# Kernel optimization log

Hardware: AMD Instinct MI355X
Metric: run time of the kernel (lower is better)

The kernel has to match this reference:

```python
import jax, jax.numpy as jnp
import numpy as np

N, F, H, F_ = 8192, 256, 2, 64
NEG_MASK = -1e10
LEAKY_SLOPE = 0.2


def setup_inputs() -> dict:
    key = jax.random.key(0)
    k0, k1, k2, k3 = jax.random.split(key, 4)
    X = jax.random.normal(k0, (N, F), jnp.float32)
    A = (jax.random.uniform(k1, (N, N)) < 0.01).astype(jnp.float32)
    A = jnp.maximum(A, jnp.eye(N, dtype=jnp.float32))
    W = jax.random.normal(k2, (H, F, F_), jnp.float32) * (1.0 / np.sqrt(F))
    b = jnp.zeros((H, F_), jnp.float32)
    a = jax.random.normal(k3, (H, F_), jnp.float32) * 0.1
    return {"X": X, "A": A, "W": W, "b": b, "a": a}


def reference(X, A, W, b, a):
    # per-head projected features: [H, N, F_]
    feats = jnp.einsum('nf,hfo->hno', X, W)
    # score[h,i,j] = sum_o feats[h,i,o] * feats[h,j,o] * a[h,o]
    # (identical math to Dot(axes=-1)([X_0*X_1, a^T]) without the [N,N,F_] tensor)
    scores = jnp.einsum('hno,hmo->hnm', feats * a[:, None, :], feats)
    scores = jax.nn.leaky_relu(scores, negative_slope=LEAKY_SLOPE)
    scores = scores + NEG_MASK * (1.0 - A)  # adjacency mask (broadcast over heads)
    attn = jax.nn.softmax(scores, axis=-1)  # [H, N, N]
    # dropout_rate=0 -> identity at inference
    out = jnp.einsum('hnm,hmo->hno', attn, feats) + b[:, None, :]  # [H, N, F_]
    out = jnp.transpose(out, (1, 0, 2)).reshape(X.shape[0], H * F_)  # concat heads
    return jax.nn.relu(out)
```

## Files before the change

kernel.cpp:

```cpp
#include <hip/hip_runtime.h>

#define NN 8192
#define FIN 256
#define FO 64
#define CAP 192

typedef float nf4 __attribute__((ext_vector_type(4)));

__global__ __launch_bounds__(256) void feats_kernel(
    const float* __restrict__ X,
    const float* __restrict__ W,
    float* __restrict__ feats)
{
    __shared__ float Ws[128*FO];
    __shared__ float Xs[32*132];
    const int h = blockIdx.y;
    const int row0 = blockIdx.x * 32;
    const int t = threadIdx.x;
    const int rg = t >> 4;
    const int c0 = (t & 15) << 2;
    float acc0[4] = {0.f,0.f,0.f,0.f};
    float acc1[4] = {0.f,0.f,0.f,0.f};

    for (int kp = 0; kp < 2; ++kp){
        const int kb = kp * 128;
        const float* Wh = W + h*FIN*FO + kb*FO;
        #pragma unroll
        for (int it=0; it<8; ++it){
            int flat = (it*256 + t)*4;
            *(float4*)&Ws[flat] = *(const float4*)&Wh[flat];
        }
        #pragma unroll
        for (int it=0; it<4; ++it){
            int flat = (it*256 + t)*4;
            int r = flat >> 7, f0 = flat & 127;
            *(float4*)&Xs[r*132 + f0] = *(const float4*)&X[(size_t)(row0+r)*FIN + kb + f0];
        }
        __syncthreads();
        const float* xp0 = &Xs[(rg*2+0)*132];
        const float* xp1 = &Xs[(rg*2+1)*132];
        #pragma unroll 4
        for (int k=0; k<128; ++k){
            float x0 = xp0[k], x1 = xp1[k];
            float4 w4 = *(const float4*)&Ws[k*FO + c0];
            acc0[0]=fmaf(x0,w4.x,acc0[0]); acc0[1]=fmaf(x0,w4.y,acc0[1]);
            acc0[2]=fmaf(x0,w4.z,acc0[2]); acc0[3]=fmaf(x0,w4.w,acc0[3]);
            acc1[0]=fmaf(x1,w4.x,acc1[0]); acc1[1]=fmaf(x1,w4.y,acc1[1]);
            acc1[2]=fmaf(x1,w4.z,acc1[2]); acc1[3]=fmaf(x1,w4.w,acc1[3]);
        }
        __syncthreads();
    }
    float* o0 = feats + ((size_t)(row0 + rg*2 + 0)*2 + h)*FO + c0;
    float* o1 = feats + ((size_t)(row0 + rg*2 + 1)*2 + h)*FO + c0;
    *(float4*)o0 = make_float4(acc0[0],acc0[1],acc0[2],acc0[3]);
    *(float4*)o1 = make_float4(acc1[0],acc1[1],acc1[2],acc1[3]);
}

__global__ __launch_bounds__(512) void gat_kernel(
    const float* __restrict__ A,
    const float* __restrict__ feats,
    const float* __restrict__ av,
    const float* __restrict__ bv,
    float* __restrict__ out)
{
    __shared__ int   nsh[CAP];
    __shared__ float s0[CAP], s1[CAP];
    __shared__ float part[8*128];
    __shared__ float red[2];
    __shared__ int   s_c;

    const int i = blockIdx.x, t = threadIdx.x;
    const int l  = t & 63;
    const int wv = t >> 6;
    const int gi = t >> 5, l32 = t & 31;

    float4 qa = *(const float4*)&av[l32*4];
    float4 qf = *(const float4*)&feats[(size_t)i*128 + l32*4];
    const float4 q4 = make_float4(qf.x*qa.x, qf.y*qa.y, qf.z*qa.z, qf.w*qa.w);

    if (t == 0) s_c = 0;
    __syncthreads();

    const nf4* Arow4 = (const nf4*)(A + (size_t)i*NN);
    nf4 v[4];
    #pragma unroll
    for (int r=0; r<4; ++r) v[r] = __builtin_nontemporal_load(&Arow4[r*512 + t]);

    const unsigned long long ltmask = (1ull << l) - 1ull;
    #pragma unroll
    for (int r=0; r<4; ++r){
        unsigned long long m0 = __ballot(v[r].x != 0.0f);
        unsigned long long m1 = __ballot(v[r].y != 0.0f);
        unsigned long long m2 = __ballot(v[r].z != 0.0f);
        unsigned long long m3 = __ballot(v[r].w != 0.0f);
        int p0 = __popcll(m0), p1 = __popcll(m1), p2 = __popcll(m2), p3 = __popcll(m3);
        int base = 0;
        if (l == 0) base = atomicAdd(&s_c, p0+p1+p2+p3);
        base = __shfl(base, 0, 64);
        const int colb = (r*512 + t)*4;
        if ((m0>>l)&1){ int p = base + __popcll(m0 & ltmask); if (p<CAP) nsh[p] = colb;   } base += p0;
        if ((m1>>l)&1){ int p = base + __popcll(m1 & ltmask); if (p<CAP) nsh[p] = colb+1; } base += p1;
        if ((m2>>l)&1){ int p = base + __popcll(m2 & ltmask); if (p<CAP) nsh[p] = colb+2; } base += p2;
        if ((m3>>l)&1){ int p = base + __popcll(m3 & ltmask); if (p<CAP) nsh[p] = colb+3; }
    }
    __syncthreads();
    const int n = min(s_c, CAP);

    for (int k0 = gi*4; k0 < n; k0 += 64){
        const int kn = min(4, n - k0);
        float4 f[4];
        #pragma unroll
        for (int u=0; u<4; ++u){
            int j = (u < kn) ? nsh[k0+u] : i;
            f[u] = *(const float4*)&feats[(size_t)j*128 + l32*4];
        }
        #pragma unroll
        for (int u=0; u<4; ++u){
            float d = f[u].x*q4.x + f[u].y*q4.y + f[u].z*q4.z + f[u].w*q4.w;
            d += __shfl_xor(d, 1, 64);
            d += __shfl_xor(d, 2, 64);
            d += __shfl_xor(d, 4, 64);
            d += __shfl_xor(d, 8, 64);
            d = (d >= 0.f) ? d : 0.2f*d;
            if (u < kn){
                if (l32 == 0)  s0[k0+u] = d;
                if (l32 == 16) s1[k0+u] = d;
            }
        }
    }
    __syncthreads();

    if (wv < 2){
        float* ss = wv ? s1 : s0;
        float m = -1e30f;
        for (int k=l; k<n; k+=64) m = fmaxf(m, ss[k]);
        #pragma unroll
        for (int off=32; off; off>>=1) m = fmaxf(m, __shfl_xor(m, off, 64));
        float sum = 0.f;
        for (int k=l; k<n; k+=64){ float p = __expf(ss[k]-m); ss[k] = p; sum += p; }
        #pragma unroll
        for (int off=32; off; off>>=1) sum += __shfl_xor(sum, off, 64);
        if (l == 0) red[wv] = sum;
    }
    __syncthreads();

    const int g8 = t >> 6;
    const int o2 = (t & 63) * 2;
    const float* ps = (o2 >= 64) ? s1 : s0;
    float2 acc = make_float2(0.f, 0.f);
    int k = g8;
    for (; k + 24 < n; k += 32){
        int j0 = nsh[k], j1 = nsh[k+8], j2 = nsh[k+16], j3 = nsh[k+24];
        float2 f0 = *(const float2*)&feats[(size_t)j0*128 + o2];
        float2 f1 = *(const float2*)&feats[(size_t)j1*128 + o2];
        float2 f2 = *(const float2*)&feats[(size_t)j2*128 + o2];
        float2 f3 = *(const float2*)&feats[(size_t)j3*128 + o2];
        float p0 = ps[k], p1 = ps[k+8], p2 = ps[k+16], p3 = ps[k+24];
        acc.x = fmaf(p0, f0.x, acc.x); acc.y = fmaf(p0, f0.y, acc.y);
        acc.x = fmaf(p1, f1.x, acc.x); acc.y = fmaf(p1, f1.y, acc.y);
        acc.x = fmaf(p2, f2.x, acc.x); acc.y = fmaf(p2, f2.y, acc.y);
        acc.x = fmaf(p3, f3.x, acc.x); acc.y = fmaf(p3, f3.y, acc.y);
    }
    for (; k < n; k += 8){
        int j = nsh[k];
        float2 f = *(const float2*)&feats[(size_t)j*128 + o2];
        float p = ps[k];
        acc.x = fmaf(p, f.x, acc.x); acc.y = fmaf(p, f.y, acc.y);
    }
    *(float2*)&part[g8*128 + o2] = acc;
    __syncthreads();

    if (t < 128){
        float num = part[t]       + part[128+t] + part[256+t] + part[384+t]
                  + part[512+t]   + part[640+t] + part[768+t] + part[896+t];
        float val = num / red[t>>6] + bv[t];
        out[(size_t)i*128 + t] = fmaxf(val, 0.f);
    }
}

extern "C" void kernel_launch(void* const* d_in, const int* in_sizes, int n_in,
                              void* d_out, int out_size, void* d_ws, size_t ws_size,
                              hipStream_t stream) {
    const float* X = (const float*)d_in[0];
    const float* A = (const float*)d_in[1];
    const float* W = (const float*)d_in[2];
    const float* b = (const float*)d_in[3];
    const float* a = (const float*)d_in[4];
    float* out = (float*)d_out;

    float* feats = (float*)d_ws;

    feats_kernel<<<dim3(NN/32, 2), 256, 0, stream>>>(X, W, feats);
    gat_kernel  <<<dim3(NN),       512, 0, stream>>>(A, feats, a, b, out);
}
```

Before: 391.9 us.

## Process four GAT rows per block and prefetch the next adjacency row

The attention kernel now handles four consecutive rows per block, using 256 threads instead of one row per 512-thread block. While the current row's neighbour list is compacted and aggregated, the block issues non-temporal loads for the next row of A into registers, so the streaming read overlaps with compute. The aggregation phase uses float4 gathers per thread to fit the smaller block. The feats output indexing is rewritten in an equivalent form. In exchange there are four times fewer blocks, fewer threads per row and more registers per thread, which can reduce the latency hiding that parallelism across blocks used to provide.

```diff
diff --git a/kernel.cpp b/kernel.cpp
--- a/kernel.cpp
+++ b/kernel.cpp
@@ -4,6 +4,7 @@
 #define FIN 256
 #define FO 64
 #define CAP 192
+#define RPB 4
 
 typedef float nf4 __attribute__((ext_vector_type(4)));
 
@@ -50,13 +51,13 @@
         }
         __syncthreads();
     }
-    float* o0 = feats + ((size_t)(row0 + rg*2 + 0)*2 + h)*FO + c0;
-    float* o1 = feats + ((size_t)(row0 + rg*2 + 1)*2 + h)*FO + c0;
+    float* o0 = feats + (size_t)(row0 + rg*2 + 0)*128 + h*FO + c0;
+    float* o1 = feats + (size_t)(row0 + rg*2 + 1)*128 + h*FO + c0;
     *(float4*)o0 = make_float4(acc0[0],acc0[1],acc0[2],acc0[3]);
     *(float4*)o1 = make_float4(acc1[0],acc1[1],acc1[2],acc1[3]);
 }
 
-__global__ __launch_bounds__(512) void gat_kernel(
+__global__ __launch_bounds__(256) void gat_kernel(
     const float* __restrict__ A,
     const float* __restrict__ feats,
     const float* __restrict__ av,
@@ -69,112 +70,125 @@
     __shared__ float red[2];
     __shared__ int   s_c;
 
-    const int i = blockIdx.x, t = threadIdx.x;
+    const int t = threadIdx.x;
     const int l  = t & 63;
     const int wv = t >> 6;
     const int gi = t >> 5, l32 = t & 31;
-
-    float4 qa = *(const float4*)&av[l32*4];
-    float4 qf = *(const float4*)&feats[(size_t)i*128 + l32*4];
-    const float4 q4 = make_float4(qf.x*qa.x, qf.y*qa.y, qf.z*qa.z, qf.w*qa.w);
+    const int base_row = blockIdx.x * RPB;
+
+    const float4 qa = *(const float4*)&av[l32*4];
+    const unsigned long long ltmask = (1ull << l) - 1ull;
 
     if (t == 0) s_c = 0;
     __syncthreads();
 
-    const nf4* Arow4 = (const nf4*)(A + (size_t)i*NN);
-    nf4 v[4];
-    #pragma unroll
-    for (int r=0; r<4; ++r) v[r] = __builtin_nontemporal_load(&Arow4[r*512 + t]);
-
-    const unsigned long long ltmask = (1ull << l) - 1ull;
-    #pragma unroll
-    for (int r=0; r<4; ++r){
-        unsigned long long m0 = __ballot(v[r].x != 0.0f);
-        unsigned long long m1 = __ballot(v[r].y != 0.0f);
-        unsigned long long m2 = __ballot(v[r].z != 0.0f);
-        unsigned long long m3 = __ballot(v[r].w != 0.0f);
-        int p0 = __popcll(m0), p1 = __popcll(m1), p2 = __popcll(m2), p3 = __popcll(m3);
-        int base = 0;
-        if (l == 0) base = atomicAdd(&s_c, p0+p1+p2+p3);
-        base = __shfl(base, 0, 64);
-        const int colb = (r*512 + t)*4;
-        if ((m0>>l)&1){ int p = base + __popcll(m0 & ltmask); if (p<CAP) nsh[p] = colb;   } base += p0;
-        if ((m1>>l)&1){ int p = base + __popcll(m1 & ltmask); if (p<CAP) nsh[p] = colb+1; } base += p1;
-        if ((m2>>l)&1){ int p = base + __popcll(m2 & ltmask); if (p<CAP) nsh[p] = colb+2; } base += p2;
-        if ((m3>>l)&1){ int p = base + __popcll(m3 & ltmask); if (p<CAP) nsh[p] = colb+3; }
+    nf4 v[8];
+    {
+        const nf4* Ar = (const nf4*)(A + (size_t)base_row*NN);
+        #pragma unroll
+        for (int r=0; r<8; ++r) v[r] = __builtin_nontemporal_load(&Ar[r*256 + t]);
     }
-    __syncthreads();
-    const int n = min(s_c, CAP);
-
-    for (int k0 = gi*4; k0 < n; k0 += 64){
-        const int kn = min(4, n - k0);
-        float4 f[4];
-        #pragma unroll
-        for (int u=0; u<4; ++u){
-            int j = (u < kn) ? nsh[k0+u] : i;
-            f[u] = *(const float4*)&feats[(size_t)j*128 + l32*4];
-        }
-        #pragma unroll
-        for (int u=0; u<4; ++u){
-            float d = f[u].x*q4.x + f[u].y*q4.y + f[u].z*q4.z + f[u].w*q4.w;
-            d += __shfl_xor(d, 1, 64);
-            d += __shfl_xor(d, 2, 64);
-            d += __shfl_xor(d, 4, 64);
-            d += __shfl_xor(d, 8, 64);
-            d = (d >= 0.f) ? d : 0.2f*d;
-            if (u < kn){
-                if (l32 == 0)  s0[k0+u] = d;
-                if (l32 == 16) s1[k0+u] = d;
+
+    for (int rr=0; rr<RPB; ++rr){
+        const int i = base_row + rr;
+
+        float4 qf = *(const float4*)&feats[(size_t)i*128 + l32*4];
+        const float4 q4 = make_float4(qf.x*qa.x, qf.y*qa.y, qf.z*qa.z, qf.w*qa.w);
+
+        #pragma unroll
+        for (int r=0; r<8; ++r){
+            unsigned long long m0 = __ballot(v[r].x != 0.0f);
+            unsigned long long m1 = __ballot(v[r].y != 0.0f);
+            unsigned long long m2 = __ballot(v[r].z != 0.0f);
+            unsigned long long m3 = __ballot(v[r].w != 0.0f);
+            int p0 = __popcll(m0), p1 = __popcll(m1), p2 = __popcll(m2), p3 = __popcll(m3);
+            int base = 0;
+            if (l == 0) base = atomicAdd(&s_c, p0+p1+p2+p3);
+            base = __shfl(base, 0, 64);
+            const int colb = (r*256 + t)*4;
+            if ((m0>>l)&1){ int p = base + __popcll(m0 & ltmask); if (p<CAP) nsh[p] = colb;   } base += p0;
+            if ((m1>>l)&1){ int p = base + __popcll(m1 & ltmask); if (p<CAP) nsh[p] = colb+1; } base += p1;
+            if ((m2>>l)&1){ int p = base + __popcll(m2 & ltmask); if (p<CAP) nsh[p] = colb+2; } base += p2;
+            if ((m3>>l)&1){ int p = base + __popcll(m3 & ltmask); if (p<CAP) nsh[p] = colb+3; }
+        }
+        if (rr < RPB-1){
+            const nf4* An = (const nf4*)(A + (size_t)(i+1)*NN);
+            #pragma unroll
+            for (int r=0; r<8; ++r) v[r] = __builtin_nontemporal_load(&An[r*256 + t]);
+        }
+        __syncthreads();
+        const int n = min(s_c, CAP);
+
+        for (int k0 = gi*4; k0 < n; k0 += 32){
+            const int kn = min(4, n - k0);
+            float4 f[4];
+            #pragma unroll
+            for (int u=0; u<4; ++u){
+                int j = (u < kn) ? nsh[k0+u] : i;
+                f[u] = *(const float4*)&feats[(size_t)j*128 + l32*4];
             }
-        }
-    }
-    __syncthreads();
-
-    if (wv < 2){
-        float* ss = wv ? s1 : s0;
-        float m = -1e30f;
-        for (int k=l; k<n; k+=64) m = fmaxf(m, ss[k]);
-        #pragma unroll
-        for (int off=32; off; off>>=1) m = fmaxf(m, __shfl_xor(m, off, 64));
-        float sum = 0.f;
-        for (int k=l; k<n; k+=64){ float p = __expf(ss[k]-m); ss[k] = p; sum += p; }
-        #pragma unroll
-        for (int off=32; off; off>>=1) sum += __shfl_xor(sum, off, 64);
-        if (l == 0) red[wv] = sum;
-    }
-    __syncthreads();
-
-    const int g8 = t >> 6;
-    const int o2 = (t & 63) * 2;
-    const float* ps = (o2 >= 64) ? s1 : s0;
-    float2 acc = make_float2(0.f, 0.f);
-    int k = g8;
-    for (; k + 24 < n; k += 32){
-        int j0 = nsh[k], j1 = nsh[k+8], j2 = nsh[k+16], j3 = nsh[k+24];
-        float2 f0 = *(const float2*)&feats[(size_t)j0*128 + o2];
-        float2 f1 = *(const float2*)&feats[(size_t)j1*128 + o2];
-        float2 f2 = *(const float2*)&feats[(size_t)j2*128 + o2];
-        float2 f3 = *(const float2*)&feats[(size_t)j3*128 + o2];
-        float p0 = ps[k], p1 = ps[k+8], p2 = ps[k+16], p3 = ps[k+24];
-        acc.x = fmaf(p0, f0.x, acc.x); acc.y = fmaf(p0, f0.y, acc.y);
-        acc.x = fmaf(p1, f1.x, acc.x); acc.y = fmaf(p1, f1.y, acc.y);
-        acc.x = fmaf(p2, f2.x, acc.x); acc.y = fmaf(p2, f2.y, acc.y);
-        acc.x = fmaf(p3, f3.x, acc.x); acc.y = fmaf(p3, f3.y, acc.y);
-    }
-    for (; k < n; k += 8){
-        int j = nsh[k];
-        float2 f = *(const float2*)&feats[(size_t)j*128 + o2];
-        float p = ps[k];
-        acc.x = fmaf(p, f.x, acc.x); acc.y = fmaf(p, f.y, acc.y);
-    }
-    *(float2*)&part[g8*128 + o2] = acc;
-    __syncthreads();
-
-    if (t < 128){
-        float num = part[t]       + part[128+t] + part[256+t] + part[384+t]
-                  + part[512+t]   + part[640+t] + part[768+t] + part[896+t];
-        float val = num / red[t>>6] + bv[t];
-        out[(size_t)i*128 + t] = fmaxf(val, 0.f);
+            #pragma unroll
+            for (int u=0; u<4; ++u){
+                float d = f[u].x*q4.x + f[u].y*q4.y + f[u].z*q4.z + f[u].w*q4.w;
+                d += __shfl_xor(d, 1, 64);
+                d += __shfl_xor(d, 2, 64);
+                d += __shfl_xor(d, 4, 64);
+                d += __shfl_xor(d, 8, 64);
+                d = (d >= 0.f) ? d : 0.2f*d;
+                if (u < kn){
+                    if (l32 == 0)  s0[k0+u] = d;
+                    if (l32 == 16) s1[k0+u] = d;
+                }
+            }
+        }
+        __syncthreads();
+
+        if (wv < 2){
+            float* ss = wv ? s1 : s0;
+            float m = -1e30f;
+            for (int k=l; k<n; k+=64) m = fmaxf(m, ss[k]);
+            #pragma unroll
+            for (int off=32; off; off>>=1) m = fmaxf(m, __shfl_xor(m, off, 64));
+            float sum = 0.f;
+            for (int k=l; k<n; k+=64){ float p = __expf(ss[k]-m); ss[k] = p; sum += p; }
+            #pragma unroll
+            for (int off=32; off; off>>=1) sum += __shfl_xor(sum, off, 64);
+            if (l == 0) red[wv] = sum;
+        }
+        if (t == 192) s_c = 0;
+        __syncthreads();
+
+        const int o4 = l32*4;
+        const float* ps = (l32 >= 16) ? s1 : s0;
+        float4 acc = make_float4(0.f,0.f,0.f,0.f);
+        int k = gi;
+        for (; k + 24 < n; k += 32){
+            int j0 = nsh[k], j1 = nsh[k+8], j2 = nsh[k+16], j3 = nsh[k+24];
+            float4 f0 = *(const float4*)&feats[(size_t)j0*128 + o4];
+            float4 f1 = *(const float4*)&feats[(size_t)j1*128 + o4];
+            float4 f2 = *(const float4*)&feats[(size_t)j2*128 + o4];
+            float4 f3 = *(const float4*)&feats[(size_t)j3*128 + o4];
+            float p0 = ps[k], p1 = ps[k+8], p2 = ps[k+16], p3 = ps[k+24];
+            acc.x=fmaf(p0,f0.x,acc.x); acc.y=fmaf(p0,f0.y,acc.y); acc.z=fmaf(p0,f0.z,acc.z); acc.w=fmaf(p0,f0.w,acc.w);
+            acc.x=fmaf(p1,f1.x,acc.x); acc.y=fmaf(p1,f1.y,acc.y); acc.z=fmaf(p1,f1.z,acc.z); acc.w=fmaf(p1,f1.w,acc.w);
+            acc.x=fmaf(p2,f2.x,acc.x); acc.y=fmaf(p2,f2.y,acc.y); acc.z=fmaf(p2,f2.z,acc.z); acc.w=fmaf(p2,f2.w,acc.w);
+            acc.x=fmaf(p3,f3.x,acc.x); acc.y=fmaf(p3,f3.y,acc.y); acc.z=fmaf(p3,f3.z,acc.z); acc.w=fmaf(p3,f3.w,acc.w);
+        }
+        for (; k < n; k += 8){
+            int j = nsh[k];
+            float4 f = *(const float4*)&feats[(size_t)j*128 + o4];
+            float p = ps[k];
+            acc.x=fmaf(p,f.x,acc.x); acc.y=fmaf(p,f.y,acc.y); acc.z=fmaf(p,f.z,acc.z); acc.w=fmaf(p,f.w,acc.w);
+        }
+        *(float4*)&part[gi*128 + o4] = acc;
+        __syncthreads();
+
+        if (t < 128){
+            float num = part[t]     + part[128+t] + part[256+t] + part[384+t]
+                      + part[512+t] + part[640+t] + part[768+t] + part[896+t];
+            float val = num / red[t>>6] + bv[t];
+            out[(size_t)i*128 + t] = fmaxf(val, 0.f);
+        }
     }
 }
 
@@ -191,5 +205,5 @@
     float* feats = (float*)d_ws;
 
     feats_kernel<<<dim3(NN/32, 2), 256, 0, stream>>>(X, W, feats);
-    gat_kernel  <<<dim3(NN),       512, 0, stream>>>(A, feats, a, b, out);
+    gat_kernel  <<<dim3(NN/RPB),   256, 0, stream>>>(A, feats, a, b, out);
 }
```

New measurement: 431.2 us. 10.0% more time.
